# Kernel optimization log

Hardware: AMD Instinct MI355X
Metric: run time of the kernel (lower is better)

## Reference

```python
import jax, jax.numpy as jnp
import numpy as np

B, L = 2, 256
H, W = 256, 128
FLAT = H * W              # 32768
D_MODEL = 1024
D_INNER = 2 * D_MODEL     # 2048
D_STATE = 16
D_CONV = 4
DT_RANK = D_MODEL // 16   # 64


def _rmsnorm(x, w, eps=1e-5):
    return x * jax.lax.rsqrt(jnp.mean(x * x, axis=-1, keepdims=True) + eps) * w


def _selective_scan(dA, dBu, C):
    # dA, dBu: (B, L, D_INNER, D_STATE); C: (B, L, D_STATE)
    def step(h, inp):
        a, bu, c = inp
        h = a * h + bu
        return h, jnp.einsum('bdn,bn->bd', h, c)
    h0 = jnp.zeros((dA.shape[0], dA.shape[2], dA.shape[3]), dA.dtype)
    _, ys = jax.lax.scan(step, h0, (jnp.swapaxes(dA, 0, 1), jnp.swapaxes(dBu, 0, 1), jnp.swapaxes(C, 0, 1)))
    return jnp.swapaxes(ys, 0, 1)  # (B, L, D_INNER)


def _mamba_block(x, norm_w, in_proj_w, conv_w, conv_b, x_proj_w, dt_proj_w, dt_proj_b, A_log, D_skip, out_proj_w):
    xn = _rmsnorm(x, norm_w)
    xz = xn @ in_proj_w.T                        # (B, L, 2*D_INNER)
    u, z = jnp.split(xz, 2, axis=-1)
    # causal depthwise conv over the sequence dim
    u = jax.lax.conv_general_dilated(u, conv_w, (1,), [(D_CONV - 1, 0)],
                                     dimension_numbers=('NWC', 'WIO', 'NWC'),
                                     feature_group_count=D_INNER) + conv_b
    u = jax.nn.silu(u)
    dbc = u @ x_proj_w.T                         # (B, L, DT_RANK + 2*D_STATE)
    dt_r, Bm, Cm = jnp.split(dbc, [DT_RANK, DT_RANK + D_STATE], axis=-1)
    dt = jax.nn.softplus(dt_r @ dt_proj_w.T + dt_proj_b)  # (B, L, D_INNER)
    A = -jnp.exp(A_log)                          # (D_INNER, D_STATE)
    dA = jnp.exp(dt[..., None] * A)              # (B, L, D_INNER, D_STATE)
    dBu = (dt * u)[..., None] * Bm[:, :, None, :]
    y = _selective_scan(dA, dBu, Cm) + D_skip * u
    y = y * jax.nn.silu(z)
    return x + y @ out_proj_w.T


def setup_inputs():
    key = jax.random.key(0)
    ks = jax.random.split(key, 12)
    g = lambda i, shape, sc: jax.random.normal(ks[i], shape, dtype=jnp.float32) * sc
    return {
        'x': (jax.random.uniform(ks[0], (B, L, H, W)) < 0.1).astype(jnp.float32),
        'enc_w': g(1, (D_MODEL, FLAT), 0.005),
        'enc_b': jnp.zeros((D_MODEL,), jnp.float32),
        'dec_w': g(2, (FLAT, D_MODEL), 0.02),
        'dec_b': jnp.zeros((FLAT,), jnp.float32),
        'norm_w': jnp.ones((D_MODEL,), jnp.float32),
        'in_proj_w': g(3, (2 * D_INNER, D_MODEL), 0.02),
        'conv_w': g(4, (D_CONV, 1, D_INNER), 0.2),
        'conv_b': jnp.zeros((D_INNER,), jnp.float32),
        'x_proj_w': g(5, (DT_RANK + 2 * D_STATE, D_INNER), 0.02),
        'dt_proj_w': g(6, (D_INNER, DT_RANK), 0.1),
        'dt_proj_b': jnp.full((D_INNER,), -2.0, jnp.float32),
        'A_log': jnp.log(jnp.tile(jnp.arange(1, D_STATE + 1, dtype=jnp.float32), (D_INNER, 1))),
        'D_skip': jnp.ones((D_INNER,), jnp.float32),
        'out_proj_w': g(7, (D_MODEL, D_INNER), 0.02),
    }


def reference(x, enc_w, enc_b, dec_w, dec_b, norm_w, in_proj_w, conv_w, conv_b,
              x_proj_w, dt_proj_w, dt_proj_b, A_log, D_skip, out_proj_w):
    b, l = x.shape[:2]
    lat = x.reshape(b, l, FLAT) @ enc_w.T + enc_b          # frozen encoder
    h = _mamba_block(lat, norm_w, in_proj_w, conv_w, conv_b, x_proj_w,
                     dt_proj_w, dt_proj_b, A_log, D_skip, out_proj_w)
    probs = jax.nn.sigmoid(h @ dec_w.T + dec_b)            # frozen decoder + sigmoid
    return probs.reshape(b, l, H, W)[:, :-1]
```

## Files before the change

### kernel.cpp

```cpp
#include <hip/hip_runtime.h>
#include <math.h>
#include <stdint.h>

#define BB 2
#define LL 256
#define FLAT 32768
#define DM 1024
#define DI 2048
#define DS 16
#define DTR 64
#define ML (BB*LL)

#define EPI_NONE 0
#define EPI_BIAS 1
#define EPI_SOFTPLUS 2
#define EPI_DEC 4

typedef __attribute__((ext_vector_type(8))) short bf16x8;
typedef __attribute__((ext_vector_type(4))) float f32x4;
typedef __attribute__((ext_vector_type(8))) unsigned short u16x8;
typedef __attribute__((ext_vector_type(4))) unsigned short u16x4;

__device__ __forceinline__ float sigmoid_f(float x) { return 1.0f / (1.0f + __expf(-x)); }

__device__ __forceinline__ unsigned short f2bf(float f) {
    unsigned u = __float_as_uint(f);
    u += 0x7fffu + ((u >> 16) & 1u);
    return (unsigned short)(u >> 16);
}

__device__ __forceinline__ void gld_lds16(const void* g, void* l) {
    __builtin_amdgcn_global_load_lds(
        (const __attribute__((address_space(1))) unsigned int*)g,
        (__attribute__((address_space(3))) unsigned int*)l, 16, 0, 0);
}

__global__ __launch_bounds__(256) void cvt_bf16_k(
    const float* __restrict__ in, unsigned short* __restrict__ out, int n8)
{
    const int i = blockIdx.x * 256 + threadIdx.x;
    if (i >= n8) return;
    const float4 a = ((const float4*)in)[2 * i];
    const float4 b = ((const float4*)in)[2 * i + 1];
    u16x8 r;
    r[0] = f2bf(a.x); r[1] = f2bf(a.y); r[2] = f2bf(a.z); r[3] = f2bf(a.w);
    r[4] = f2bf(b.x); r[5] = f2bf(b.y); r[6] = f2bf(b.z); r[7] = f2bf(b.w);
    ((u16x8*)out)[i] = r;
}

template<int EPI, bool SPLIT>
__global__ __launch_bounds__(256) void gemm_bf16(
    const unsigned short* __restrict__ A, const unsigned short* __restrict__ B,
    float* __restrict__ C, int M, int N, int K, int lda, int ldb, int kChunk,
    const float* __restrict__ bias)
{
    __shared__ __align__(16) char lds[32768];

    const int t  = threadIdx.x;
    const int w  = t >> 6;
    const int l  = t & 63;
    const int m0 = blockIdx.x * 128;
    const int n0 = blockIdx.y * 128;
    const int wr = w >> 1, wc = w & 1;

    int kb = 0, ke = K;
    float* Cout = C;
    if (SPLIT) { kb = blockIdx.z * kChunk; ke = kb + kChunk;
                 Cout = C + (size_t)blockIdx.z * M * N; }

    const int srow0 = w * 32 + (l >> 3);
    const int ssub  = l & 7;

    f32x4 acc[4][4];
#pragma unroll
    for (int i = 0; i < 4; ++i)
#pragma unroll
        for (int j = 0; j < 4; ++j) acc[i][j] = (f32x4){0.f, 0.f, 0.f, 0.f};

    const int lr = l & 15, h = l >> 4;

    for (int kt = kb; kt < ke; kt += 64) {
#pragma unroll
        for (int q = 0; q < 4; ++q) {
            const int row = srow0 + q * 8;
            gld_lds16(A + (size_t)(m0 + row) * lda + kt + ((ssub ^ (row & 7)) << 3),
                      lds + w * 4096 + q * 1024);
        }
#pragma unroll
        for (int q = 0; q < 4; ++q) {
            const int row = srow0 + q * 8;
            gld_lds16(B + (size_t)(n0 + row) * ldb + kt + ((ssub ^ (row & 7)) << 3),
                      lds + 16384 + w * 4096 + q * 1024);
        }
        __syncthreads();

#pragma unroll
        for (int ks = 0; ks < 2; ++ks) {
            bf16x8 af[4], bfr[4];
#pragma unroll
            for (int i = 0; i < 4; ++i) {
                const int r = wr * 64 + i * 16 + lr;
                const int sub = (ks * 4 + h) ^ (r & 7);
                af[i] = *(const bf16x8*)(lds + r * 128 + sub * 16);
            }
#pragma unroll
            for (int j = 0; j < 4; ++j) {
                const int c = wc * 64 + j * 16 + lr;
                const int sub = (ks * 4 + h) ^ (c & 7);
                bfr[j] = *(const bf16x8*)(lds + 16384 + c * 128 + sub * 16);
            }
#pragma unroll
            for (int i = 0; i < 4; ++i)
#pragma unroll
                for (int j = 0; j < 4; ++j)
                    acc[i][j] = __builtin_amdgcn_mfma_f32_16x16x32_bf16(
                        af[i], bfr[j], acc[i][j], 0, 0, 0);
        }
        __syncthreads();
    }

#pragma unroll
    for (int i = 0; i < 4; ++i)
#pragma unroll
        for (int j = 0; j < 4; ++j)
#pragma unroll
            for (int rg = 0; rg < 4; ++rg) {
                const int row = m0 + wr * 64 + i * 16 + h * 4 + rg;
                const int col = n0 + wc * 64 + j * 16 + lr;
                float v = acc[i][j][rg];
                if (SPLIT || EPI == EPI_NONE) {
                    Cout[(size_t)row * N + col] = v;
                } else if (EPI == EPI_DEC) {
                    v = sigmoid_f(v + bias[col]);
                    const int b = row >> 8, ll = row & 255;
                    if (ll < 255) Cout[(((size_t)(b * 255 + ll)) << 15) + col] = v;
                }
            }
}

template<int EPI, bool SPLIT>
__global__ __launch_bounds__(256) void gemm_nt(
    const float* __restrict__ A, const float* __restrict__ B,
    float* __restrict__ C, int M, int N, int K, int lda, int ldb,
    int kChunk, const float* __restrict__ bias)
{
    __shared__ float As[32][64];
    __shared__ float Bs[32][64];

    const int m0 = blockIdx.x * 64;
    const int n0 = blockIdx.y * 64;
    const int t  = threadIdx.x;

    int kb = 0, ke = K;
    float* Cout = C;
    if (SPLIT) { kb = blockIdx.z * kChunk; ke = kb + kChunk; Cout = C + (size_t)blockIdx.z * M * N; }

    const int lrow = t >> 3;
    const int lcol = (t & 7) << 2;

    float acc[4][4];
#pragma unroll
    for (int i = 0; i < 4; ++i)
#pragma unroll
        for (int j = 0; j < 4; ++j) acc[i][j] = 0.0f;

    const int tx = t & 15, ty = t >> 4;

    for (int k = kb; k < ke; k += 32) {
#pragma unroll
        for (int i = 0; i < 2; ++i) {
            const int row = lrow + i * 32;
            float4 av = *(const float4*)&A[(m0 + row) * lda + k + lcol];
            As[lcol + 0][row] = av.x; As[lcol + 1][row] = av.y;
            As[lcol + 2][row] = av.z; As[lcol + 3][row] = av.w;
            const int nn = n0 + row;
            float4 bv = make_float4(0.f, 0.f, 0.f, 0.f);
            if (nn < N) bv = *(const float4*)&B[nn * ldb + k + lcol];
            Bs[lcol + 0][row] = bv.x; Bs[lcol + 1][row] = bv.y;
            Bs[lcol + 2][row] = bv.z; Bs[lcol + 3][row] = bv.w;
        }
        __syncthreads();
#pragma unroll
        for (int kk = 0; kk < 32; ++kk) {
            float4 a4 = *(const float4*)&As[kk][ty << 2];
            float4 b4 = *(const float4*)&Bs[kk][tx << 2];
            const float a[4] = { a4.x, a4.y, a4.z, a4.w };
            const float b[4] = { b4.x, b4.y, b4.z, b4.w };
#pragma unroll
            for (int i = 0; i < 4; ++i)
#pragma unroll
                for (int j = 0; j < 4; ++j)
                    acc[i][j] = fmaf(a[i], b[j], acc[i][j]);
        }
        __syncthreads();
    }

#pragma unroll
    for (int i = 0; i < 4; ++i) {
        const int m = m0 + (ty << 2) + i;
#pragma unroll
        for (int j = 0; j < 4; ++j) {
            const int n = n0 + (tx << 2) + j;
            if (n >= N) continue;
            float v = acc[i][j];
            if (SPLIT || EPI == EPI_NONE) {
                Cout[m * N + n] = v;
            } else if (EPI == EPI_SOFTPLUS) {
                v += bias[n];
                Cout[m * N + n] = fmaxf(v, 0.0f) + log1pf(__expf(-fabsf(v)));
            }
        }
    }
}

template<int EPI>
__global__ __launch_bounds__(256) void splitk_reduce(
    const float* __restrict__ part, float* __restrict__ C,
    int MN, int N, int S, const float* __restrict__ bias)
{
    const int i = blockIdx.x * 256 + threadIdx.x;
    if (i >= MN) return;
    float s = 0.0f;
    for (int j = 0; j < S; ++j) s += part[(size_t)j * MN + i];
    if (EPI == EPI_BIAS) s += bias[i % N];
    C[i] = s;
}

__global__ __launch_bounds__(256) void splitk_reduce_resid_bf16(
    const float* __restrict__ part, const float* __restrict__ resid,
    unsigned short* __restrict__ outb, int MN, int S)
{
    const int i = blockIdx.x * 256 + threadIdx.x;
    if (i >= MN) return;
    float s = 0.0f;
    for (int j = 0; j < S; ++j) s += part[(size_t)j * MN + i];
    outb[i] = f2bf(s + resid[i]);
}

__global__ __launch_bounds__(256) void rmsnorm_k(
    const float* __restrict__ x, const float* __restrict__ w,
    unsigned short* __restrict__ o)
{
    const int row = blockIdx.x;
    const int t = threadIdx.x;
    const float* xr = x + row * DM;
    float4 xv = *(const float4*)&xr[t * 4];
    float ss = xv.x * xv.x + xv.y * xv.y + xv.z * xv.z + xv.w * xv.w;
#pragma unroll
    for (int off = 32; off > 0; off >>= 1) ss += __shfl_xor(ss, off);
    __shared__ float red[4];
    if ((t & 63) == 0) red[t >> 6] = ss;
    __syncthreads();
    const float tot = red[0] + red[1] + red[2] + red[3];
    const float scale = rsqrtf(tot * (1.0f / DM) + 1e-5f);
    float4 wv = *(const float4*)&w[t * 4];
    u16x4 ov;
    ov[0] = f2bf(xv.x * scale * wv.x); ov[1] = f2bf(xv.y * scale * wv.y);
    ov[2] = f2bf(xv.z * scale * wv.z); ov[3] = f2bf(xv.w * scale * wv.w);
    *(u16x4*)&o[row * DM + t * 4] = ov;
}

__global__ __launch_bounds__(256) void conv_silu_k(
    const float* __restrict__ xz, const float* __restrict__ cw,
    const float* __restrict__ cb, float* __restrict__ u)
{
    const int idx = blockIdx.x * 256 + threadIdx.x;
    if (idx >= ML * DI) return;
    const int d  = idx & (DI - 1);
    const int bl = idx >> 11;
    const int l  = bl & (LL - 1);
    float s = cb[d];
#pragma unroll
    for (int w = 0; w < 4; ++w) {
        const int ls = l - 3 + w;
        if (ls >= 0) s = fmaf(xz[(bl - 3 + w) * (2 * DI) + d], cw[w * DI + d], s);
    }
    u[idx] = s * sigmoid_f(s);
}

__global__ __launch_bounds__(256) void scan_k(
    const float* __restrict__ dt, const float* __restrict__ u,
    const float* __restrict__ xz, const float* __restrict__ dbc,
    const float* __restrict__ A_log, const float* __restrict__ Dskip,
    unsigned short* __restrict__ y)
{
    const int t = blockIdx.x * 256 + threadIdx.x;
    const int n  = t & (DS - 1);
    const int ch = t >> 4;
    const int d  = ch & (DI - 1);
    const int b  = ch >> 11;
    const float a  = -__expf(A_log[d * DS + n]);
    const float Dv = Dskip[d];
    float h = 0.0f;
    const int rbase = b * LL;

    for (int l0 = 0; l0 < LL; l0 += 8) {
        float dtv[8], uv[8], Bv[8], Cv[8], zv[8];
#pragma unroll
        for (int s = 0; s < 8; ++s) {
            const int r = rbase + l0 + s;
            dtv[s] = dt[r * DI + d];
            uv[s]  = u[r * DI + d];
            Bv[s]  = dbc[r * 96 + DTR + n];
            Cv[s]  = dbc[r * 96 + DTR + DS + n];
            zv[s]  = xz[r * (2 * DI) + DI + d];
        }
        float p[8];
#pragma unroll
        for (int s = 0; s < 8; ++s) {
            const float dA = __expf(dtv[s] * a);
            h = fmaf(dA, h, dtv[s] * uv[s] * Bv[s]);
            p[s] = h * Cv[s];
        }
#pragma unroll
        for (int s = 0; s < 8; ++s) p[s] += __shfl_xor(p[s], 1);
#pragma unroll
        for (int s = 0; s < 8; ++s) p[s] += __shfl_xor(p[s], 2);
#pragma unroll
        for (int s = 0; s < 8; ++s) p[s] += __shfl_xor(p[s], 4);
#pragma unroll
        for (int s = 0; s < 8; ++s) p[s] += __shfl_xor(p[s], 8);
        if (n == 0) {
#pragma unroll
            for (int s = 0; s < 8; ++s) {
                const int r = rbase + l0 + s;
                const float yy = fmaf(Dv, uv[s], p[s]);
                y[r * DI + d] = f2bf(yy * zv[s] * sigmoid_f(zv[s]));
            }
        }
    }
}

extern "C" void kernel_launch(void* const* d_in, const int* in_sizes, int n_in,
                              void* d_out, int out_size, void* d_ws, size_t ws_size,
                              hipStream_t stream)
{
    const float* x        = (const float*)d_in[0];
    const float* enc_w    = (const float*)d_in[1];
    const float* enc_b    = (const float*)d_in[2];
    const float* dec_w    = (const float*)d_in[3];
    const float* dec_b    = (const float*)d_in[4];
    const float* norm_w   = (const float*)d_in[5];
    const float* in_proj  = (const float*)d_in[6];
    const float* conv_w   = (const float*)d_in[7];
    const float* conv_b   = (const float*)d_in[8];
    const float* x_proj   = (const float*)d_in[9];
    const float* dt_projw = (const float*)d_in[10];
    const float* dt_projb = (const float*)d_in[11];
    const float* A_log    = (const float*)d_in[12];
    const float* D_skip   = (const float*)d_in[13];
    const float* out_proj = (const float*)d_in[14];
    float* out = (float*)d_out;
    (void)in_sizes; (void)n_in; (void)out_size; (void)ws_size;

    char* wsb = (char*)d_ws;
    unsigned short* wbf = (unsigned short*)(wsb);
    float* part = (float*)(wsb + 67108864);
    float* lat  = (float*)(wsb + 100663296);
    float* dt   = (float*)(wsb + 102760448);
    char* S0 = wsb + 106954752;
    unsigned short* xbf    = (unsigned short*)(S0);
    unsigned short* inpbf  = (unsigned short*)(S0);
    unsigned short* outpbf = (unsigned short*)(S0 + 8388608);
    unsigned short* xnbf   = (unsigned short*)(S0 + 12582912);
    unsigned short* ybf    = (unsigned short*)(S0 + 13631488);
    unsigned short* houtbf = (unsigned short*)(S0 + 15728640);
    float* xz  = (float*)(S0 + 16777216);
    float* u   = (float*)(S0 + 25165824);
    float* dbc = (float*)(S0 + 29360128);

    cvt_bf16_k<<<(FLAT * ML / 8) / 256, 256, 0, stream>>>(x, xbf, FLAT * ML / 8);
    cvt_bf16_k<<<(DM * FLAT / 8) / 256, 256, 0, stream>>>(enc_w, wbf, DM * FLAT / 8);

    {
        dim3 g(ML / 128, DM / 128, 16);
        gemm_bf16<EPI_NONE, true><<<g, 256, 0, stream>>>(xbf, wbf, part, ML, DM, FLAT,
                                                         FLAT, FLAT, FLAT / 16, nullptr);
        splitk_reduce<EPI_BIAS><<<(ML * DM) / 256, 256, 0, stream>>>(part, lat, ML * DM, DM, 16, enc_b);
    }

    rmsnorm_k<<<ML, 256, 0, stream>>>(lat, norm_w, xnbf);

    cvt_bf16_k<<<(2 * DI * DM / 8) / 256, 256, 0, stream>>>(in_proj, inpbf, 2 * DI * DM / 8);
    {
        dim3 g(ML / 128, (2 * DI) / 128);
        gemm_bf16<EPI_NONE, false><<<g, 256, 0, stream>>>(xnbf, inpbf, xz, ML, 2 * DI, DM,
                                                          DM, DM, 0, nullptr);
    }

    conv_silu_k<<<(ML * DI) / 256, 256, 0, stream>>>(xz, conv_w, conv_b, u);

    {
        dim3 g(ML / 64, 2, 16);
        gemm_nt<EPI_NONE, true><<<g, 256, 0, stream>>>(u, x_proj, part, ML, 96, DI, DI, DI,
                                                       DI / 16, nullptr);
        splitk_reduce<EPI_NONE><<<(ML * 96 + 255) / 256, 256, 0, stream>>>(part, dbc, ML * 96, 96, 16, nullptr);
    }

    {
        dim3 g(ML / 64, DI / 64);
        gemm_nt<EPI_SOFTPLUS, false><<<g, 256, 0, stream>>>(dbc, dt_projw, dt, ML, DI, DTR,
                                                            96, DTR, 0, dt_projb);
    }

    scan_k<<<(BB * DI * DS) / 256, 256, 0, stream>>>(dt, u, xz, dbc, A_log, D_skip, ybf);

    cvt_bf16_k<<<(DM * DI / 8) / 256, 256, 0, stream>>>(out_proj, outpbf, DM * DI / 8);
    {
        dim3 g(ML / 128, DM / 128, 8);
        gemm_bf16<EPI_NONE, true><<<g, 256, 0, stream>>>(ybf, outpbf, part, ML, DM, DI,
                                                         DI, DI, DI / 8, nullptr);
        splitk_reduce_resid_bf16<<<(ML * DM) / 256, 256, 0, stream>>>(part, lat, houtbf, ML * DM, 8);
    }

    cvt_bf16_k<<<(FLAT * DM / 8) / 256, 256, 0, stream>>>(dec_w, wbf, FLAT * DM / 8);
    {
        dim3 g(ML / 128, FLAT / 128);
        gemm_bf16<EPI_DEC, false><<<g, 256, 0, stream>>>(houtbf, wbf, out, ML, FLAT, DM,
                                                         DM, DM, 0, dec_b);
    }
}
```

Baseline: 645.9 us.

## Fuse fp32-to-bf16 weight conversion into GEMM B-tile loads

Removes the separate weight conversion kernels for enc_w, in_proj, out_proj and dec_w. The GEMM now loads fp32 weight tiles straight into LDS with a 16-way XOR swizzle and converts them to bf16 with v_cvt_pk_bf16_f32 when reading fragments. This saves a full read and write of each weight matrix to workspace, but doubles the LDS footprint and B-tile load traffic inside the GEMM. The encoder split-K is also raised from 16 to 32, which doubles the partial-sum buffer that the reduction has to read.

Measured after the change: 634.6 us. Within noise of the previous version (-1.8%).

```diff
diff --git a/kernel.cpp b/kernel.cpp
--- a/kernel.cpp
+++ b/kernel.cpp
@@ -29,6 +29,12 @@
     return (unsigned short)(u >> 16);
 }
 
+__device__ __forceinline__ unsigned cvt_pk_bf16(float a, float b) {
+    unsigned r;
+    asm("v_cvt_pk_bf16_f32 %0, %1, %2" : "=v"(r) : "v"(a), "v"(b));
+    return r;
+}
+
 __device__ __forceinline__ void gld_lds16(const void* g, void* l) {
     __builtin_amdgcn_global_load_lds(
         (const __attribute__((address_space(1))) unsigned int*)g,
@@ -48,13 +54,16 @@
     ((u16x8*)out)[i] = r;
 }
 
-template<int EPI, bool SPLIT>
+template<int EPI, bool SPLIT, bool BF32>
 __global__ __launch_bounds__(256) void gemm_bf16(
-    const unsigned short* __restrict__ A, const unsigned short* __restrict__ B,
+    const unsigned short* __restrict__ A, const void* __restrict__ Bv,
     float* __restrict__ C, int M, int N, int K, int lda, int ldb, int kChunk,
     const float* __restrict__ bias)
 {
-    __shared__ __align__(16) char lds[32768];
+    __shared__ __align__(16) char lds[BF32 ? 49152 : 32768];
+
+    const float*          Bf = (const float*)Bv;
+    const unsigned short* Bh = (const unsigned short*)Bv;
 
     const int t  = threadIdx.x;
     const int w  = t >> 6;
@@ -70,6 +79,8 @@
 
     const int srow0 = w * 32 + (l >> 3);
     const int ssub  = l & 7;
+    const int brow0 = w * 32 + (l >> 4);
+    const int bgl   = l & 15;
 
     f32x4 acc[4][4];
 #pragma unroll
@@ -86,11 +97,20 @@
             gld_lds16(A + (size_t)(m0 + row) * lda + kt + ((ssub ^ (row & 7)) << 3),
                       lds + w * 4096 + q * 1024);
         }
-#pragma unroll
-        for (int q = 0; q < 4; ++q) {
-            const int row = srow0 + q * 8;
-            gld_lds16(B + (size_t)(n0 + row) * ldb + kt + ((ssub ^ (row & 7)) << 3),
-                      lds + 16384 + w * 4096 + q * 1024);
+        if (BF32) {
+#pragma unroll
+            for (int q = 0; q < 8; ++q) {
+                const int row = brow0 + q * 4;
+                gld_lds16(Bf + (size_t)(n0 + row) * ldb + kt + ((bgl ^ (row & 15)) << 2),
+                          lds + 16384 + w * 8192 + q * 1024);
+            }
+        } else {
+#pragma unroll
+            for (int q = 0; q < 4; ++q) {
+                const int row = srow0 + q * 8;
+                gld_lds16(Bh + (size_t)(n0 + row) * ldb + kt + ((ssub ^ (row & 7)) << 3),
+                          lds + 16384 + w * 4096 + q * 1024);
+            }
         }
         __syncthreads();
 
@@ -106,8 +126,21 @@
 #pragma unroll
             for (int j = 0; j < 4; ++j) {
                 const int c = wc * 64 + j * 16 + lr;
-                const int sub = (ks * 4 + h) ^ (c & 7);
-                bfr[j] = *(const bf16x8*)(lds + 16384 + c * 128 + sub * 16);
+                if (BF32) {
+                    const int g0 = (2 * (ks * 4 + h))     ^ (c & 15);
+                    const int g1 = (2 * (ks * 4 + h) + 1) ^ (c & 15);
+                    const f32x4 v0 = *(const f32x4*)(lds + 16384 + c * 256 + g0 * 16);
+                    const f32x4 v1 = *(const f32x4*)(lds + 16384 + c * 256 + g1 * 16);
+                    union { unsigned u[4]; bf16x8 v; } cv;
+                    cv.u[0] = cvt_pk_bf16(v0[0], v0[1]);
+                    cv.u[1] = cvt_pk_bf16(v0[2], v0[3]);
+                    cv.u[2] = cvt_pk_bf16(v1[0], v1[1]);
+                    cv.u[3] = cvt_pk_bf16(v1[2], v1[3]);
+                    bfr[j] = cv.v;
+                } else {
+                    const int sub = (ks * 4 + h) ^ (c & 7);
+                    bfr[j] = *(const bf16x8*)(lds + 16384 + c * 128 + sub * 16);
+                }
             }
 #pragma unroll
             for (int i = 0; i < 4; ++i)
@@ -354,38 +387,33 @@
     (void)in_sizes; (void)n_in; (void)out_size; (void)ws_size;
 
     char* wsb = (char*)d_ws;
-    unsigned short* wbf = (unsigned short*)(wsb);
-    float* part = (float*)(wsb + 67108864);
-    float* lat  = (float*)(wsb + 100663296);
-    float* dt   = (float*)(wsb + 102760448);
-    char* S0 = wsb + 106954752;
+    float* part = (float*)(wsb);
+    float* lat  = (float*)(wsb + 67108864);
+    float* dt   = (float*)(wsb + 69206016);
+    char* S0 = wsb + 73400320;
     unsigned short* xbf    = (unsigned short*)(S0);
-    unsigned short* inpbf  = (unsigned short*)(S0);
-    unsigned short* outpbf = (unsigned short*)(S0 + 8388608);
-    unsigned short* xnbf   = (unsigned short*)(S0 + 12582912);
-    unsigned short* ybf    = (unsigned short*)(S0 + 13631488);
-    unsigned short* houtbf = (unsigned short*)(S0 + 15728640);
-    float* xz  = (float*)(S0 + 16777216);
-    float* u   = (float*)(S0 + 25165824);
-    float* dbc = (float*)(S0 + 29360128);
+    unsigned short* xnbf   = (unsigned short*)(S0);
+    unsigned short* ybf    = (unsigned short*)(S0 + 1048576);
+    unsigned short* houtbf = (unsigned short*)(S0 + 3145728);
+    float* xz  = (float*)(S0 + 4194304);
+    float* u   = (float*)(S0 + 12582912);
+    float* dbc = (float*)(S0 + 16777216);
 
     cvt_bf16_k<<<(FLAT * ML / 8) / 256, 256, 0, stream>>>(x, xbf, FLAT * ML / 8);
-    cvt_bf16_k<<<(DM * FLAT / 8) / 256, 256, 0, stream>>>(enc_w, wbf, DM * FLAT / 8);
-
-    {
-        dim3 g(ML / 128, DM / 128, 16);
-        gemm_bf16<EPI_NONE, true><<<g, 256, 0, stream>>>(xbf, wbf, part, ML, DM, FLAT,
-                                                         FLAT, FLAT, FLAT / 16, nullptr);
-        splitk_reduce<EPI_BIAS><<<(ML * DM) / 256, 256, 0, stream>>>(part, lat, ML * DM, DM, 16, enc_b);
+
+    {
+        dim3 g(ML / 128, DM / 128, 32);
+        gemm_bf16<EPI_NONE, true, true><<<g, 256, 0, stream>>>(
+            xbf, enc_w, part, ML, DM, FLAT, FLAT, FLAT, FLAT / 32, nullptr);
+        splitk_reduce<EPI_BIAS><<<(ML * DM) / 256, 256, 0, stream>>>(part, lat, ML * DM, DM, 32, enc_b);
     }
 
     rmsnorm_k<<<ML, 256, 0, stream>>>(lat, norm_w, xnbf);
 
-    cvt_bf16_k<<<(2 * DI * DM / 8) / 256, 256, 0, stream>>>(in_proj, inpbf, 2 * DI * DM / 8);
     {
         dim3 g(ML / 128, (2 * DI) / 128);
-        gemm_bf16<EPI_NONE, false><<<g, 256, 0, stream>>>(xnbf, inpbf, xz, ML, 2 * DI, DM,
-                                                          DM, DM, 0, nullptr);
+        gemm_bf16<EPI_NONE, false, true><<<g, 256, 0, stream>>>(
+            xnbf, in_proj, xz, ML, 2 * DI, DM, DM, DM, 0, nullptr);
     }
 
     conv_silu_k<<<(ML * DI) / 256, 256, 0, stream>>>(xz, conv_w, conv_b, u);
@@ -405,18 +433,16 @@
 
     scan_k<<<(BB * DI * DS) / 256, 256, 0, stream>>>(dt, u, xz, dbc, A_log, D_skip, ybf);
 
-    cvt_bf16_k<<<(DM * DI / 8) / 256, 256, 0, stream>>>(out_proj, outpbf, DM * DI / 8);
     {
         dim3 g(ML / 128, DM / 128, 8);
-        gemm_bf16<EPI_NONE, true><<<g, 256, 0, stream>>>(ybf, outpbf, part, ML, DM, DI,
-                                                         DI, DI, DI / 8, nullptr);
+        gemm_bf16<EPI_NONE, true, true><<<g, 256, 0, stream>>>(
+            ybf, out_proj, part, ML, DM, DI, DI, DI, DI / 8, nullptr);
         splitk_reduce_resid_bf16<<<(ML * DM) / 256, 256, 0, stream>>>(part, lat, houtbf, ML * DM, 8);
     }
 
-    cvt_bf16_k<<<(FLAT * DM / 8) / 256, 256, 0, stream>>>(dec_w, wbf, FLAT * DM / 8);
     {
         dim3 g(ML / 128, FLAT / 128);
-        gemm_bf16<EPI_DEC, false><<<g, 256, 0, stream>>>(houtbf, wbf, out, ML, FLAT, DM,
-                                                         DM, DM, 0, dec_b);
-    }
-}
+        gemm_bf16<EPI_DEC, false, true><<<g, 256, 0, stream>>>(
+            houtbf, dec_w, out, ML, FLAT, DM, DM, DM, 0, dec_b);
+    }
+}
```
